# Performance work log

Hardware: AMD Instinct MI355X
Metric: run time of the kernel (lower is better)

The kernel has to match this reference:

```python
import jax, jax.numpy as jnp
import numpy as np

D_TOTAL, H, D_HEAD, HID = 2048, 16, 128, 512
EPS = float(np.finfo(np.float32).eps)  # nn.RMSNorm eps=None -> dtype eps


def _xavier(key, shape):
    # xavier_uniform over last two dims (per-head init)
    fan_in, fan_out = shape[-2], shape[-1]
    limit = float(np.sqrt(6.0 / (fan_in + fan_out)))
    return jax.random.uniform(key, shape, jnp.float32, -limit, limit)


def setup_inputs() -> dict:
    key = jax.random.key(0)
    ks = jax.random.split(key, 6)
    x = jax.random.normal(ks[0], (4, 4096, D_TOTAL), jnp.float32)
    g = jnp.ones((D_TOTAL,), jnp.float32)  # RMSNorm weight
    w0 = _xavier(ks[1], (H, D_HEAD, HID))
    w1 = _xavier(ks[2], (H, HID, HID))
    w2 = _xavier(ks[3], (H, HID, HID))
    w3 = _xavier(ks[4], (H, HID, D_HEAD))
    return {"x": x, "g": g, "w0": w0, "w1": w1, "w2": w2, "w3": w3}


def _rms_norm(x, g):
    var = jnp.mean(jnp.square(x), axis=-1, keepdims=True)
    return x * jax.lax.rsqrt(var + EPS) * g


def reference(x, g, w0, w1, w2, w3):
    h = _rms_norm(x, g)
    lead = h.shape[:-1]
    hp = h.reshape(*lead, H, D_HEAD)  # (B,S,H,d_head)
    gelu = lambda t: jax.nn.gelu(t, approximate=False)
    hp = jnp.einsum('bshd,hde->bshe', hp, w0)
    hp = jnp.einsum('bshd,hde->bshe', gelu(hp), w1)
    hp = jnp.einsum('bshd,hde->bshe', gelu(hp), w2)
    hp = jnp.einsum('bshd,hde->bshe', gelu(hp), w3)
    return hp.reshape(*lead, D_TOTAL)
```

## Files before the change

kernel.cpp:

```cpp
#include <hip/hip_runtime.h>
#include <cstdint>
#include <cstddef>

#define N_TOK   16384
#define D_TOTAL 2048
#define N_HEAD  16
#define D_HEAD  128
#define HID     512
#define MT      128
#define RMS_EPS 1.1920929e-07f

typedef __attribute__((ext_vector_type(8)))  short  short8;
typedef __attribute__((ext_vector_type(4)))  float  float4_t;
typedef __attribute__((ext_vector_type(16))) float  f32x16;
typedef __attribute__((ext_vector_type(2)))  unsigned int uint2_t;

__device__ __forceinline__ unsigned short f2bf(float f) {
    union { float f; unsigned int i; } v; v.f = f;
    unsigned int b = v.i;
    b += 0x7FFFu + ((b >> 16) & 1u);
    return (unsigned short)(b >> 16);
}

__device__ __forceinline__ unsigned int cvt_pk_bf16(float lo, float hi) {
    unsigned int r;
    asm("v_cvt_pk_bf16_f32 %0, %1, %2" : "=v"(r) : "v"(lo), "v"(hi));
    return r;
}

__device__ __forceinline__ float fast_exp2(float x) {
#if __has_builtin(__builtin_amdgcn_exp2f)
    return __builtin_amdgcn_exp2f(x);
#else
    return exp2f(x);
#endif
}

__device__ __forceinline__ float gelu_exact(float x) {
    float ax = fabsf(x);
    float t  = __builtin_amdgcn_rcpf(fmaf(0.23164193f, ax, 1.0f));
    float poly = fmaf(fmaf(fmaf(fmaf(1.061405429f, t, -1.453152027f),
                               t, 1.421413741f), t, -0.284496736f),
                      t, 0.254829592f) * t;
    float e    = fast_exp2(x * x * -0.72134752f);
    float erfa = fmaf(-poly, e, 1.0f);
    return fmaf(0.5f * ax, erfa, 0.5f * x);
}

__global__ __launch_bounds__(256) void prep_kernel(
    const float* __restrict__ x, float* __restrict__ scale,
    const float* __restrict__ w0, const float* __restrict__ w1,
    const float* __restrict__ w2, const float* __restrict__ w3,
    const float* __restrict__ gw,
    unsigned short* __restrict__ wt0, unsigned short* __restrict__ wt1,
    unsigned short* __restrict__ wt2, unsigned short* __restrict__ wt3)
{
    int b = blockIdx.x;
    if (b < 4096) {
        const int lane  = threadIdx.x & 63;
        const int wv    = threadIdx.x >> 6;
        const int token = b * 4 + wv;
        const float* xp = x + (size_t)token * D_TOTAL;
        float s = 0.0f;
#pragma unroll
        for (int j = 0; j < 8; ++j) {
            float4 v = *(const float4*)(xp + (size_t)(j * 64 + lane) * 4);
            s += v.x * v.x + v.y * v.y + v.z * v.z + v.w * v.w;
        }
#pragma unroll
        for (int off = 32; off > 0; off >>= 1) s += __shfl_down(s, off, 64);
        if (lane == 0)
            scale[token] = rsqrtf(s * (1.0f / (float)D_TOTAL) + RMS_EPS);
        return;
    }

    b -= 4096;
    const float* in; unsigned short* out; int K, N; const float* gm = nullptr;
    if      (b <  256) { in = w0; out = wt0; K = 128; N = 512; gm = gw; }
    else if (b < 1280) { in = w1; out = wt1; K = 512; N = 512; b -= 256; }
    else if (b < 2304) { in = w2; out = wt2; K = 512; N = 512; b -= 1280; }
    else               { in = w3; out = wt3; K = 512; N = 128; b -= 2304; }

    const int ktiles = K >> 6, ntiles = N >> 6;
    const int h   = b / (ktiles * ntiles);
    const int rem = b % (ktiles * ntiles);
    const int kt  = rem / ntiles, nt = rem % ntiles;

    const float* src = in + (size_t)h * K * N + (size_t)(kt * 64) * N + nt * 64;
    unsigned short* dst = out + (size_t)h * N * K + (size_t)(nt * 64) * K + kt * 64;

    __shared__ unsigned short tile[64][72];

#pragma unroll
    for (int p = 0; p < 2; ++p) {
        int gi = threadIdx.x + p * 256;
        int r  = gi >> 3;
        int gc = (gi & 7) * 8;
        float mul = 1.0f;
        if (gm) mul = gm[(size_t)h * K + kt * 64 + r];
        float4 a  = *(const float4*)(src + (size_t)r * N + gc);
        float4 b4 = *(const float4*)(src + (size_t)r * N + gc + 4);
        unsigned short tmp[8];
        tmp[0]=f2bf(a.x*mul);  tmp[1]=f2bf(a.y*mul);  tmp[2]=f2bf(a.z*mul);  tmp[3]=f2bf(a.w*mul);
        tmp[4]=f2bf(b4.x*mul); tmp[5]=f2bf(b4.y*mul); tmp[6]=f2bf(b4.z*mul); tmp[7]=f2bf(b4.w*mul);
        *(uint4*)&tile[r][gc] = *(const uint4*)tmp;
    }
    __syncthreads();
#pragma unroll
    for (int p = 0; p < 2; ++p) {
        int gi  = threadIdx.x + p * 256;
        int r2  = gi >> 3;
        int gc2 = (gi & 7) * 8;
        unsigned short tmp[8];
#pragma unroll
        for (int j = 0; j < 8; ++j) tmp[j] = tile[gc2 + j][r2];
        *(uint4*)(dst + (size_t)r2 * K + gc2) = *(const uint4*)tmp;
    }
}

template<int K, int MTT, int NT>
__device__ __forceinline__ void stage_gemm32(
    const unsigned short* __restrict__ sA,
    const unsigned short* __restrict__ wt,
    int lane, int mt0, int nbase, f32x16 acc[MTT][NT])
{
    constexpr int NK = K / 16;
#pragma unroll
    for (int mt = 0; mt < MTT; ++mt)
#pragma unroll
        for (int nt = 0; nt < NT; ++nt)
#pragma unroll
            for (int i = 0; i < 16; ++i) acc[mt][nt][i] = 0.0f;

    const int r31 = lane & 31;
    const int h   = lane >> 5;

    const char* arow[NT];
#pragma unroll
    for (int nt = 0; nt < NT; ++nt)
        arow[nt] = (const char*)(wt + (size_t)(nbase + nt * 32 + r31) * K + h * 8);

    const char* sab = (const char*)sA;
    unsigned int vb[MTT];
#pragma unroll
    for (int mt = 0; mt < MTT; ++mt) {
        unsigned int row = (unsigned)(mt0 + mt * 32 + r31);
        unsigned int r7  = row & 7u;
        unsigned int g0  = (r7 & 6u) | ((unsigned)h ^ (r7 & 1u));
        vb[mt] = row * 1024u + (g0 << 4);
    }

    short8 apf[2][NT];
#pragma unroll
    for (int nt = 0; nt < NT; ++nt) apf[0][nt] = *(const short8*)(arow[nt]);
#pragma unroll
    for (int nt = 0; nt < NT; ++nt) apf[1][nt] = *(const short8*)(arow[nt] + 32);

#pragma unroll
    for (int ks = 0; ks < NK; ++ks) {
        short8 a[NT];
#pragma unroll
        for (int nt = 0; nt < NT; ++nt) a[nt] = apf[ks & 1][nt];
        if (ks + 2 < NK) {
#pragma unroll
            for (int nt = 0; nt < NT; ++nt)
                apf[ks & 1][nt] = *(const short8*)(arow[nt] + (ks + 2) * 32);
        }
        short8 b[MTT];
#pragma unroll
        for (int mt = 0; mt < MTT; ++mt)
            b[mt] = *(const short8*)(sab + (vb[mt] ^ (unsigned)(ks << 5)));
#pragma unroll
        for (int mt = 0; mt < MTT; ++mt)
#pragma unroll
            for (int nt = 0; nt < NT; ++nt)
                acc[mt][nt] = __builtin_amdgcn_mfma_f32_32x32x16_bf16(
                    a[nt], b[mt], acc[mt][nt], 0, 0, 0);
    }
}

template<int MTT, int NT>
__device__ __forceinline__ void epi_gelu32(
    unsigned short* __restrict__ sAct, int lane, int mt0, int nbase,
    f32x16 acc[MTT][NT])
{
    const int r31 = lane & 31;
    const int h   = lane >> 5;
#pragma unroll
    for (int mt = 0; mt < MTT; ++mt) {
        const int tok = mt0 + mt * 32 + r31;
        const unsigned int rbase = (unsigned)tok * HID;
        const int tk7 = tok & 7;
#pragma unroll
        for (int nt = 0; nt < NT; ++nt)
#pragma unroll
            for (int g = 0; g < 4; ++g) {
                const int col = nbase + nt * 32 + 8 * g + 4 * h;
                float g0 = gelu_exact(acc[mt][nt][4 * g + 0]);
                float g1 = gelu_exact(acc[mt][nt][4 * g + 1]);
                float g2 = gelu_exact(acc[mt][nt][4 * g + 2]);
                float g3 = gelu_exact(acc[mt][nt][4 * g + 3]);
                uint2_t v;
                v.x = cvt_pk_bf16(g0, g1);
                v.y = cvt_pk_bf16(g2, g3);
                const int gsw = (col >> 3) ^ tk7;
                *(uint2_t*)&sAct[rbase + gsw * 8 + (col & 7)] = v;
            }
    }
}

__global__ __launch_bounds__(512, 2) void fused_chain_kernel(
    const float*          __restrict__ x,
    const float*          __restrict__ scale,
    const unsigned short* __restrict__ wt0,
    const unsigned short* __restrict__ wt1,
    const unsigned short* __restrict__ wt2,
    const unsigned short* __restrict__ wt3,
    float*                __restrict__ out)
{
    __shared__ unsigned short sAct[MT * HID];

    const int tid  = threadIdx.x;
    const int lane = tid & 63;
    const int wv   = tid >> 6;
    const int bx    = blockIdx.x;
    const int xcd   = bx & 7;
    const int local = bx >> 3;
    const int head  = xcd * 2 + (local >> 7);
    const int tile  = local & 127;
    const int tok0  = tile * MT;

#pragma unroll
    for (int p = 0; p < 4; ++p) {
        int gi = tid + p * 512;
        int r  = gi >> 4;
        int gc = gi & 15;
        int token = tok0 + r;
        const float* xp = x + (size_t)token * D_TOTAL + head * D_HEAD + gc * 8;
        float4 xa = *(const float4*)(xp);
        float4 xb = *(const float4*)(xp + 4);
        float s = scale[token];
        unsigned int u[4];
        u[0] = cvt_pk_bf16(xa.x * s, xa.y * s);
        u[1] = cvt_pk_bf16(xa.z * s, xa.w * s);
        u[2] = cvt_pk_bf16(xb.x * s, xb.y * s);
        u[3] = cvt_pk_bf16(xb.z * s, xb.w * s);
        int gsw = gc ^ (r & 7);
        *(uint4*)&sAct[r * HID + gsw * 8] = *(const uint4*)u;
    }
    __syncthreads();

    f32x16 acc[4][2];
    const int nb = wv * 64;

    stage_gemm32<128, 4, 2>(sAct, wt0 + (size_t)head * HID * D_HEAD, lane, 0, nb, acc);
    __syncthreads();
    epi_gelu32<4, 2>(sAct, lane, 0, nb, acc);
    __syncthreads();

    stage_gemm32<512, 4, 2>(sAct, wt1 + (size_t)head * HID * HID, lane, 0, nb, acc);
    __syncthreads();
    epi_gelu32<4, 2>(sAct, lane, 0, nb, acc);
    __syncthreads();

    stage_gemm32<512, 4, 2>(sAct, wt2 + (size_t)head * HID * HID, lane, 0, nb, acc);
    __syncthreads();
    epi_gelu32<4, 2>(sAct, lane, 0, nb, acc);
    __syncthreads();

    const int nt4 = (wv & 3) * 32;
    const int mt4 = (wv >> 2) * 64;
    f32x16 acc2[2][1];
    stage_gemm32<512, 2, 1>(sAct, wt3 + (size_t)head * D_HEAD * HID, lane, mt4, nt4, acc2);

    const int r31 = lane & 31;
    const int h   = lane >> 5;
#pragma unroll
    for (int mt = 0; mt < 2; ++mt) {
        const int token = tok0 + mt4 + mt * 32 + r31;
#pragma unroll
        for (int g = 0; g < 4; ++g) {
            const int col = head * D_HEAD + nt4 + 8 * g + 4 * h;
            float4_t v;
            v[0] = acc2[mt][0][4 * g + 0];
            v[1] = acc2[mt][0][4 * g + 1];
            v[2] = acc2[mt][0][4 * g + 2];
            v[3] = acc2[mt][0][4 * g + 3];
            *(float4_t*)&out[(size_t)token * D_TOTAL + col] = v;
        }
    }
}

extern "C" void kernel_launch(void* const* d_in, const int* in_sizes, int n_in,
                              void* d_out, int out_size, void* d_ws, size_t ws_size,
                              hipStream_t stream)
{
    const float* x  = (const float*)d_in[0];
    const float* gw = (const float*)d_in[1];
    const float* w0 = (const float*)d_in[2];
    const float* w1 = (const float*)d_in[3];
    const float* w2 = (const float*)d_in[4];
    const float* w3 = (const float*)d_in[5];
    float* out = (float*)d_out;

    float* scale = (float*)d_ws;
    unsigned short* wt0 = (unsigned short*)((char*)d_ws + 65536);
    unsigned short* wt1 = wt0 + (size_t)N_HEAD * HID * D_HEAD;
    unsigned short* wt2 = wt1 + (size_t)N_HEAD * HID * HID;
    unsigned short* wt3 = wt2 + (size_t)N_HEAD * HID * HID;

    prep_kernel<<<4096 + 2560, 256, 0, stream>>>(
        x, scale, w0, w1, w2, w3, gw, wt0, wt1, wt2, wt3);

    fused_chain_kernel<<<N_HEAD * (N_TOK / MT), 512, 0, stream>>>(
        x, scale, wt0, wt1, wt2, wt3, out);
}
```

Baseline: 824.9 us.

## Split token tile into two halves and interleave GELU epilogues with MFMA loops

Splits the 128-token tile into two 64-token halves with separate accumulators and LDS buffers. While one half's GEMM runs, the other half's GELU epilogue and bf16 stores are interleaved into the k-loop through a callback, and the second half's input load happens during the first half's stage-0 GEMM. The goal is to hide the transcendental GELU work and stage-0 global loads behind matrix-core execution instead of running them serially between barriers. In exchange, each wave does only 2x2 MFMA tiles per k-step, so weight reuse per load halves and the weights are streamed from L2 twice as often.

New measurement: 957.2 us. +16.0%, slower.

```diff
diff --git a/kernel.cpp b/kernel.cpp
--- a/kernel.cpp
+++ b/kernel.cpp
@@ -8,6 +8,7 @@
 #define D_HEAD  128
 #define HID     512
 #define MT      128
+#define HT      64
 #define RMS_EPS 1.1920929e-07f
 
 typedef __attribute__((ext_vector_type(8)))  short  short8;
@@ -118,11 +119,52 @@
     }
 }
 
-template<int K, int MTT, int NT>
+__device__ __forceinline__ void epi_group(
+    unsigned short* __restrict__ sH, int lane, const f32x16 (&acc)[2][2],
+    int nbase, int gi)
+{
+    const int r31 = lane & 31;
+    const int h   = lane >> 5;
+    const int mt  = gi >> 3, nt = (gi >> 2) & 1, g = gi & 3;
+    const int tok = mt * 32 + r31;
+    const int col = nbase + nt * 32 + 8 * g + 4 * h;
+    float g0 = gelu_exact(acc[mt][nt][4 * g + 0]);
+    float g1 = gelu_exact(acc[mt][nt][4 * g + 1]);
+    float g2 = gelu_exact(acc[mt][nt][4 * g + 2]);
+    float g3 = gelu_exact(acc[mt][nt][4 * g + 3]);
+    uint2_t v;
+    v.x = cvt_pk_bf16(g0, g1);
+    v.y = cvt_pk_bf16(g2, g3);
+    const int gsw = (col >> 3) ^ (tok & 7);
+    *(uint2_t*)&sH[(unsigned)tok * HID + gsw * 8 + (col & 7)] = v;
+}
+
+__device__ __forceinline__ void stage0_chunk(
+    const float* __restrict__ x, const float* __restrict__ scale,
+    unsigned short* __restrict__ sH, int head, int tokbase, int tid, int c)
+{
+    int gi = tid + c * 512;
+    int r  = gi >> 4;
+    int gc = gi & 15;
+    int token = tokbase + r;
+    const float* xp = x + (size_t)token * D_TOTAL + head * D_HEAD + gc * 8;
+    float4 xa = *(const float4*)(xp);
+    float4 xb = *(const float4*)(xp + 4);
+    float s = scale[token];
+    unsigned int u[4];
+    u[0] = cvt_pk_bf16(xa.x * s, xa.y * s);
+    u[1] = cvt_pk_bf16(xa.z * s, xa.w * s);
+    u[2] = cvt_pk_bf16(xb.x * s, xb.y * s);
+    u[3] = cvt_pk_bf16(xb.z * s, xb.w * s);
+    int gsw = gc ^ (r & 7);
+    *(uint4*)&sH[r * HID + gsw * 8] = *(const uint4*)u;
+}
+
+template<int K, int MTT, int NT, class CB>
 __device__ __forceinline__ void stage_gemm32(
     const unsigned short* __restrict__ sA,
     const unsigned short* __restrict__ wt,
-    int lane, int mt0, int nbase, f32x16 acc[MTT][NT])
+    int lane, int mt0, int nbase, f32x16 acc[MTT][NT], CB&& cb)
 {
     constexpr int NK = K / 16;
 #pragma unroll
@@ -170,42 +212,13 @@
 #pragma unroll
         for (int mt = 0; mt < MTT; ++mt)
             b[mt] = *(const short8*)(sab + (vb[mt] ^ (unsigned)(ks << 5)));
+        cb(ks);
 #pragma unroll
         for (int mt = 0; mt < MTT; ++mt)
 #pragma unroll
             for (int nt = 0; nt < NT; ++nt)
                 acc[mt][nt] = __builtin_amdgcn_mfma_f32_32x32x16_bf16(
                     a[nt], b[mt], acc[mt][nt], 0, 0, 0);
-    }
-}
-
-template<int MTT, int NT>
-__device__ __forceinline__ void epi_gelu32(
-    unsigned short* __restrict__ sAct, int lane, int mt0, int nbase,
-    f32x16 acc[MTT][NT])
-{
-    const int r31 = lane & 31;
-    const int h   = lane >> 5;
-#pragma unroll
-    for (int mt = 0; mt < MTT; ++mt) {
-        const int tok = mt0 + mt * 32 + r31;
-        const unsigned int rbase = (unsigned)tok * HID;
-        const int tk7 = tok & 7;
-#pragma unroll
-        for (int nt = 0; nt < NT; ++nt)
-#pragma unroll
-            for (int g = 0; g < 4; ++g) {
-                const int col = nbase + nt * 32 + 8 * g + 4 * h;
-                float g0 = gelu_exact(acc[mt][nt][4 * g + 0]);
-                float g1 = gelu_exact(acc[mt][nt][4 * g + 1]);
-                float g2 = gelu_exact(acc[mt][nt][4 * g + 2]);
-                float g3 = gelu_exact(acc[mt][nt][4 * g + 3]);
-                uint2_t v;
-                v.x = cvt_pk_bf16(g0, g1);
-                v.y = cvt_pk_bf16(g2, g3);
-                const int gsw = (col >> 3) ^ tk7;
-                *(uint2_t*)&sAct[rbase + gsw * 8 + (col & 7)] = v;
-            }
     }
 }
 
@@ -218,7 +231,7 @@
     const unsigned short* __restrict__ wt3,
     float*                __restrict__ out)
 {
-    __shared__ unsigned short sAct[MT * HID];
+    __shared__ unsigned short sAct[2][HT * HID];
 
     const int tid  = threadIdx.x;
     const int lane = tid & 63;
@@ -230,62 +243,87 @@
     const int tile  = local & 127;
     const int tok0  = tile * MT;
 
-#pragma unroll
-    for (int p = 0; p < 4; ++p) {
-        int gi = tid + p * 512;
-        int r  = gi >> 4;
-        int gc = gi & 15;
-        int token = tok0 + r;
-        const float* xp = x + (size_t)token * D_TOTAL + head * D_HEAD + gc * 8;
-        float4 xa = *(const float4*)(xp);
-        float4 xb = *(const float4*)(xp + 4);
-        float s = scale[token];
-        unsigned int u[4];
-        u[0] = cvt_pk_bf16(xa.x * s, xa.y * s);
-        u[1] = cvt_pk_bf16(xa.z * s, xa.w * s);
-        u[2] = cvt_pk_bf16(xb.x * s, xb.y * s);
-        u[3] = cvt_pk_bf16(xb.z * s, xb.w * s);
-        int gsw = gc ^ (r & 7);
-        *(uint4*)&sAct[r * HID + gsw * 8] = *(const uint4*)u;
-    }
-    __syncthreads();
-
-    f32x16 acc[4][2];
+    unsigned short* sA0 = sAct[0];
+    unsigned short* sA1 = sAct[1];
+    const unsigned short* w0h = wt0 + (size_t)head * HID * D_HEAD;
+    const unsigned short* w1h = wt1 + (size_t)head * HID * HID;
+    const unsigned short* w2h = wt2 + (size_t)head * HID * HID;
+    const unsigned short* w3h = wt3 + (size_t)head * D_HEAD * HID;
+
+    f32x16 accA[2][2], accB[2][2];
     const int nb = wv * 64;
 
-    stage_gemm32<128, 4, 2>(sAct, wt0 + (size_t)head * HID * D_HEAD, lane, 0, nb, acc);
-    __syncthreads();
-    epi_gelu32<4, 2>(sAct, lane, 0, nb, acc);
-    __syncthreads();
-
-    stage_gemm32<512, 4, 2>(sAct, wt1 + (size_t)head * HID * HID, lane, 0, nb, acc);
-    __syncthreads();
-    epi_gelu32<4, 2>(sAct, lane, 0, nb, acc);
-    __syncthreads();
-
-    stage_gemm32<512, 4, 2>(sAct, wt2 + (size_t)head * HID * HID, lane, 0, nb, acc);
-    __syncthreads();
-    epi_gelu32<4, 2>(sAct, lane, 0, nb, acc);
-    __syncthreads();
-
-    const int nt4 = (wv & 3) * 32;
-    const int mt4 = (wv >> 2) * 64;
-    f32x16 acc2[2][1];
-    stage_gemm32<512, 2, 1>(sAct, wt3 + (size_t)head * D_HEAD * HID, lane, mt4, nt4, acc2);
-
-    const int r31 = lane & 31;
-    const int h   = lane >> 5;
-#pragma unroll
-    for (int mt = 0; mt < 2; ++mt) {
-        const int token = tok0 + mt4 + mt * 32 + r31;
+    stage0_chunk(x, scale, sA0, head, tok0, tid, 0);
+    stage0_chunk(x, scale, sA0, head, tok0, tid, 1);
+    __syncthreads();
+
+    stage_gemm32<128, 2, 2>(sA0, w0h, lane, 0, nb, accA, [&](int ks) {
+        if (ks == 2) stage0_chunk(x, scale, sA1, head, tok0 + HT, tid, 0);
+        if (ks == 5) stage0_chunk(x, scale, sA1, head, tok0 + HT, tid, 1);
+    });
+    __syncthreads();
+
+    stage_gemm32<128, 2, 2>(sA1, w0h, lane, 0, nb, accB, [&](int ks) {
+        epi_group(sA0, lane, accA, nb, 2 * ks);
+        epi_group(sA0, lane, accA, nb, 2 * ks + 1);
+    });
+    __syncthreads();
+
+    stage_gemm32<512, 2, 2>(sA0, w1h, lane, 0, nb, accA, [&](int ks) {
+        if (ks & 1) epi_group(sA1, lane, accB, nb, ks >> 1);
+    });
+    __syncthreads();
+
+    stage_gemm32<512, 2, 2>(sA1, w1h, lane, 0, nb, accB, [&](int ks) {
+        if (ks & 1) epi_group(sA0, lane, accA, nb, ks >> 1);
+    });
+    __syncthreads();
+
+    stage_gemm32<512, 2, 2>(sA0, w2h, lane, 0, nb, accA, [&](int ks) {
+        if (ks & 1) epi_group(sA1, lane, accB, nb, ks >> 1);
+    });
+    __syncthreads();
+
+    stage_gemm32<512, 2, 2>(sA1, w2h, lane, 0, nb, accB, [&](int ks) {
+        if (ks & 1) epi_group(sA0, lane, accA, nb, ks >> 1);
+    });
+    __syncthreads();
+
+    const int mt4 = (wv >> 2) * 32;
+    const int nb4 = (wv & 3) * 32;
+    f32x16 acc4[1][1];
+    stage_gemm32<512, 1, 1>(sA0, w3h, lane, mt4, nb4, acc4, [&](int ks) {
+        if (ks & 1) epi_group(sA1, lane, accB, nb, ks >> 1);
+    });
+
+    {
+        const int r31 = lane & 31, h = lane >> 5;
+        const int token = tok0 + mt4 + r31;
 #pragma unroll
         for (int g = 0; g < 4; ++g) {
-            const int col = head * D_HEAD + nt4 + 8 * g + 4 * h;
+            const int col = head * D_HEAD + nb4 + 8 * g + 4 * h;
             float4_t v;
-            v[0] = acc2[mt][0][4 * g + 0];
-            v[1] = acc2[mt][0][4 * g + 1];
-            v[2] = acc2[mt][0][4 * g + 2];
-            v[3] = acc2[mt][0][4 * g + 3];
+            v[0] = acc4[0][0][4 * g + 0];
+            v[1] = acc4[0][0][4 * g + 1];
+            v[2] = acc4[0][0][4 * g + 2];
+            v[3] = acc4[0][0][4 * g + 3];
+            *(float4_t*)&out[(size_t)token * D_TOTAL + col] = v;
+        }
+    }
+    __syncthreads();
+
+    stage_gemm32<512, 1, 1>(sA1, w3h, lane, mt4, nb4, acc4, [](int) {});
+    {
+        const int r31 = lane & 31, h = lane >> 5;
+        const int token = tok0 + HT + mt4 + r31;
+#pragma unroll
+        for (int g = 0; g < 4; ++g) {
+            const int col = head * D_HEAD + nb4 + 8 * g + 4 * h;
+            float4_t v;
+            v[0] = acc4[0][0][4 * g + 0];
+            v[1] = acc4[0][0][4 * g + 1];
+            v[2] = acc4[0][0][4 * g + 2];
+            v[3] = acc4[0][0][4 * g + 3];
             *(float4_t*)&out[(size_t)token * D_TOTAL + col] = v;
         }
     }
```
